# Performance work log

Hardware: AMD Instinct MI355X
Metric: run time of the kernel (lower is better)

Reference implementation:

```python
import jax, jax.numpy as jnp
import numpy as np

D_MODEL = 768
BATCH = 4096
RANK_DIST = [(4, 512), (8, 256), (16, 128), (32, 64), (64, 32)]


@jax.custom_vjp
def jumprelu(x):
    # hard threshold at 0 in fwd; full straight-through estimator in bwd
    return x * (x > 0.0).astype(x.dtype)


def _jr_fwd(x):
    return jumprelu(x), None


def _jr_bwd(res, g):
    return (g,)


jumprelu.defvjp(_jr_fwd, _jr_bwd)


def setup_inputs() -> dict:
    key = jax.random.key(0)
    keys = jax.random.split(key, 1 + 3 * len(RANK_DIST))
    inp = {"x": jax.random.normal(keys[0], (BATCH, D_MODEL), dtype=jnp.float32)}
    for i, (n, r) in enumerate(RANK_DIST):
        kV, kU, kE = keys[1 + 3 * i], keys[2 + 3 * i], keys[3 + 3 * i]
        scale = (1.0 / (D_MODEL * r)) ** 0.25
        inp[f"V{i}"] = scale * jax.random.normal(kV, (n, r, D_MODEL), dtype=jnp.float32)
        inp[f"U{i}"] = scale * jax.random.normal(kU, (n, D_MODEL, r), dtype=jnp.float32)
        enc = jax.random.normal(kE, (n, D_MODEL), dtype=jnp.float32)
        inp[f"enc{i}"] = enc / jnp.linalg.norm(enc, axis=1, keepdims=True)
        inp[f"b{i}"] = jnp.full((n,), -1.0, dtype=jnp.float32)
    return inp


def _group_forward(x, V, U, enc, b):
    n, r, d = V.shape
    pre = x @ enc.T - b                      # (b, n)
    gate = jumprelu(pre)                     # (b, n)
    Vx = jnp.einsum("nrd,bd->nbr", V, x)    # (n, b, r)
    # fused: UVx gated by gate then summed over transforms n
    out = jnp.einsum("ndr,nbr,bn->bd", U, Vx, gate)  # (b, d)
    u_norms = jnp.linalg.norm(U.reshape(n, -1), axis=1)
    v_norms = jnp.linalg.norm(V.reshape(n, -1), axis=1)
    frob = u_norms * v_norms / jnp.sqrt(jnp.asarray(d * r, dtype=x.dtype))
    return out, gate, frob


def reference(x, V0, U0, enc0, b0, V1, U1, enc1, b1, V2, U2, enc2, b2,
              V3, U3, enc3, b3, V4, U4, enc4, b4):
    Vs = [V0, V1, V2, V3, V4]
    Us = [U0, U1, U2, U3, U4]
    encs = [enc0, enc1, enc2, enc3, enc4]
    bs = [b0, b1, b2, b3, b4]
    output = jnp.zeros_like(x)
    total_sparsity = jnp.asarray(0.0, dtype=x.dtype)
    total_active = jnp.asarray(0.0, dtype=x.dtype)
    gate_acts = []
    for V, U, enc, b in zip(Vs, Us, encs, bs):
        g_out, gate, frob = _group_forward(x, V, U, enc, b)
        output = output + g_out
        mean_abs_gate = jnp.abs(gate).mean(axis=0)
        total_sparsity = total_sparsity + (jnp.tanh(mean_abs_gate) * frob).sum()
        total_active = total_active + (gate > 0).astype(x.dtype).sum(axis=1).mean()
        gate_acts.append(gate)
    return (output, total_sparsity, total_active, *gate_acts)
```

## Files before the change

kernel.cpp:

```cpp
#include <hip/hip_runtime.h>

#define BATCH 4096
#define DM 768
#define LTOT 10240
#define NG 124

typedef __bf16 bf16x8 __attribute__((ext_vector_type(8)));
typedef short short8 __attribute__((ext_vector_type(8)));
typedef float f32x4 __attribute__((ext_vector_type(4)));

struct Ptr5 { const float* p[5]; };

__device__ __forceinline__ unsigned short f2bf(float f) {
    unsigned u = __builtin_bit_cast(unsigned, f);
    unsigned r = (u + 0x7FFFu + ((u >> 16) & 1u)) >> 16;
    return (unsigned short)r;
}

__device__ __forceinline__ short8 pack8(float4 a, float4 b) {
    union { unsigned short u[8]; short8 s; } o;
    o.u[0] = f2bf(a.x); o.u[1] = f2bf(a.y); o.u[2] = f2bf(a.z); o.u[3] = f2bf(a.w);
    o.u[4] = f2bf(b.x); o.u[5] = f2bf(b.y); o.u[6] = f2bf(b.z); o.u[7] = f2bf(b.w);
    return o.s;
}


__global__ __launch_bounds__(256) void prep_k(const float* __restrict__ x,
                                              Ptr5 vp, Ptr5 up, Ptr5 ep, Ptr5 bp,
                                              unsigned short* __restrict__ vb,
                                              unsigned short* __restrict__ w2t,
                                              unsigned short* __restrict__ xb,
                                              float* __restrict__ gate_ws,
                                              float* __restrict__ outg,
                                              float* __restrict__ vslot,
                                              float* __restrict__ uslot,
                                              float* __restrict__ gslot,
                                              float* __restrict__ aslot) {
    const int basen[5] = {0, 4, 12, 28, 60};
    int bx = blockIdx.x;
    int tid = threadIdx.x;
    if (bx < 32) {
        __shared__ unsigned short lA[128 * 64];
        __shared__ unsigned short lB[128 * 64];
        __shared__ float sgs[128];
        __shared__ float sac;
        int wave = tid >> 6, lane = tid & 63;
        int wm = wave >> 1, wn = wave & 1;
        int lan15 = lane & 15, quad = lane >> 4;
        int sw = lan15 & 7;
        int m0 = bx * 128;
        f32x4 acc[4][4] = {};
        for (int k0 = 0; k0 < DM; k0 += 64) {
            __syncthreads();
            #pragma unroll
            for (int i = 0; i < 4; i++) {
                int gidx = i * 256 + tid;
                int row = gidx >> 3, kb = gidx & 7;
                int r7 = row & 7;
                int la = (row >> 3) * 512 + r7 * 64 + (kb ^ r7) * 8;
                int sidx = (m0 + row) * 192 + (k0 >> 2) + kb * 2;
                float4 a0 = ((const float4*)x)[sidx];
                float4 a1 = ((const float4*)x)[sidx + 1];
                *(short8*)(lA + la) = pack8(a0, a1);
                float4 b0 = {0.f, 0.f, 0.f, 0.f}, b1 = {0.f, 0.f, 0.f, 0.f};
                if (row < NG) {
                    int g = (row < 4) ? 0 : (row < 12) ? 1 : (row < 28) ? 2 :
                            (row < 60) ? 3 : 4;
                    int ni = row - basen[g];
                    int eidx = ni * 192 + (k0 >> 2) + kb * 2;
                    b0 = ((const float4*)ep.p[g])[eidx];
                    b1 = ((const float4*)ep.p[g])[eidx + 1];
                }
                *(short8*)(lB + la) = pack8(b0, b1);
            }
            __syncthreads();
            #pragma unroll
            for (int kk = 0; kk < 2; kk++) {
                int kb = kk * 4 + quad;
                int kel = (kb ^ sw) * 8;
                bf16x8 af[4], bfr[4];
                #pragma unroll
                for (int t = 0; t < 4; t++) {
                    short8 ra = *(const short8*)(lA + (wm * 64 + t * 16 + lan15) * 64 + kel);
                    short8 rb = *(const short8*)(lB + (wn * 64 + t * 16 + lan15) * 64 + kel);
                    af[t]  = __builtin_bit_cast(bf16x8, ra);
                    bfr[t] = __builtin_bit_cast(bf16x8, rb);
                }
                #pragma unroll
                for (int mt = 0; mt < 4; mt++)
                    #pragma unroll
                    for (int nt = 0; nt < 4; nt++)
                        acc[mt][nt] = __builtin_amdgcn_mfma_f32_16x16x32_bf16(
                            af[mt], bfr[nt], acc[mt][nt], 0, 0, 0);
            }
        }
        if (tid < 128) sgs[tid] = 0.f;
        if (tid == 0) sac = 0.f;
        __syncthreads();
        const size_t baseg[5] = {3145730ull, 3145730ull + 16384, 3145730ull + 49152,
                                 3145730ull + 114688, 3145730ull + 245760};
        float cnt = 0.f;
        #pragma unroll
        for (int nt = 0; nt < 4; nt++) {
            int col = wn * 64 + nt * 16 + lan15;
            float cs = 0.f;
            if (col < NG) {
                int g = (col < 4) ? 0 : (col < 12) ? 1 : (col < 28) ? 2 :
                        (col < 60) ? 3 : 4;
                int ni = col - basen[g];
                int w = 4 << g;
                float bv = bp.p[g][ni];
                #pragma unroll
                for (int mt = 0; mt < 4; mt++) {
                    int r0 = m0 + wm * 64 + mt * 16 + quad * 4;
                    #pragma unroll
                    for (int rg = 0; rg < 4; rg++) {
                        float pre = acc[mt][nt][rg] - bv;
                        float gt = pre > 0.f ? pre : 0.f;
                        gate_ws[(size_t)(r0 + rg) * NG + col] = gt;
                        outg[baseg[g] + (size_t)(r0 + rg) * w + ni] = gt;
                        cs += gt;
                        if (pre > 0.f) cnt += 1.f;
                    }
                }
                cs += __shfl_xor(cs, 16);
                cs += __shfl_xor(cs, 32);
                if (quad == 0) atomicAdd(&sgs[col], cs);
            }
        }
        #pragma unroll
        for (int off = 32; off > 0; off >>= 1) cnt += __shfl_xor(cnt, off);
        if (lane == 0) atomicAdd(&sac, cnt);
        __syncthreads();
        if (tid < NG) gslot[bx * NG + tid] = sgs[tid];
        if (tid == 0) aslot[bx] = sac;
    } else if (bx < 1952) {
        __shared__ float swave[4];
        int cb = bx - 32;
        int isV = cb < 960;
        int wb = isV ? cb : cb - 960;
        int g = wb / 192;
        int within = wb - g * 192;
        const float* src = isV ? vp.p[g] : up.p[g];
        int r = 512 >> g, lr = 9 - g;
        float ss = 0.f;
        #pragma unroll
        for (int i = 0; i < 8; i++) {
            int j = within * 2048 + i * 256 + tid;
            float4 v = ((const float4*)src)[j];
            ss += v.x*v.x + v.y*v.y + v.z*v.z + v.w*v.w;
            ushort4 o;
            o.x = f2bf(v.x); o.y = f2bf(v.y); o.z = f2bf(v.z); o.w = f2bf(v.w);
            if (isV) {
                ((ushort4*)vb)[(size_t)(g * 192 + within) * 2048 + i * 256 + tid] = o;
            } else {
                int idx = j * 4;
                int rr = idx & (r - 1);
                int t2 = idx >> lr;
                int d  = t2 % DM;
                int n  = t2 / DM;
                size_t dst = (size_t)d * LTOT + (size_t)(g << 11) + (size_t)n * r + rr;
                *(ushort4*)(w2t + dst) = o;
            }
        }
        #pragma unroll
        for (int off = 32; off > 0; off >>= 1) ss += __shfl_down(ss, off);
        if ((tid & 63) == 0) swave[tid >> 6] = ss;
        __syncthreads();
        if (tid == 0) {
            float t = (swave[0] + swave[1]) + (swave[2] + swave[3]);
            (isV ? vslot : uslot)[wb] = t;
        }
    } else {
        int base = (bx - 1952) * 2048;
        #pragma unroll
        for (int i = 0; i < 8; i++) {
            int j = base + i * 256 + tid;
            float4 v = ((const float4*)x)[j];
            ushort4 o;
            o.x = f2bf(v.x); o.y = f2bf(v.y); o.z = f2bf(v.z); o.w = f2bf(v.w);
            ((ushort4*)xb)[j] = o;
        }
    }
}

template <int ROWS, int NT>
__device__ __forceinline__ void stage(const unsigned short* __restrict__ src, int ld,
                                      unsigned short* lds, int wv, int lane) {
    int rsub = lane >> 3;
    int colb = ((lane ^ rsub) & 7) * 8;
    #pragma unroll
    for (int i = 0; i < ROWS * 8 / NT; i++) {
        int c = i * (NT / 64) + wv;
        const unsigned short* gp = src + (size_t)(c * 8 + rsub) * ld + colb;
        __builtin_amdgcn_global_load_lds((const __attribute__((address_space(1))) void*)gp,
                                         (__attribute__((address_space(3))) void*)(lds + c * 512),
                                         16, 0, 0);
    }
}

template <int BM, int BN, int NT>
__global__ __launch_bounds__(NT) void gemm_nt(const unsigned short* __restrict__ A,
                                              const unsigned short* __restrict__ Bm,
                                              int Kblk, int lda, int ldb,
                                              void* __restrict__ Cout,
                                              const float* __restrict__ gate, int ldc) {
    __shared__ unsigned short lA[BM * 64];
    __shared__ unsigned short lB[BN * 64];
    int tid = threadIdx.x, wave = tid >> 6, lane = tid & 63;
    constexpr int WN = BN / 64;
    int wm = wave / WN, wn = wave % WN;
    int m0 = blockIdx.x * BM, n0 = blockIdx.y * BN;
    A  += (size_t)m0 * lda;
    Bm += (size_t)n0 * ldb;
    f32x4 acc[4][4] = {};
    int lan15 = lane & 15, quad = lane >> 4;
    int sw = lan15 & 7;

    for (int k0 = 0; k0 < Kblk; k0 += 64) {
        stage<BM, NT>(A + k0, lda, lA, wave, lane);
        stage<BN, NT>(Bm + k0, ldb, lB, wave, lane);
        __syncthreads();
        #pragma unroll
        for (int kk = 0; kk < 2; kk++) {
            int kb = kk * 4 + quad;
            int kel = (kb ^ sw) * 8;
            bf16x8 af[4], bfr[4];
            #pragma unroll
            for (int t = 0; t < 4; t++) {
                short8 ra = *(const short8*)(lA + (size_t)(wm * 64 + t * 16 + lan15) * 64 + kel);
                short8 rb = *(const short8*)(lB + (size_t)(wn * 64 + t * 16 + lan15) * 64 + kel);
                af[t]  = __builtin_bit_cast(bf16x8, ra);
                bfr[t] = __builtin_bit_cast(bf16x8, rb);
            }
            #pragma unroll
            for (int mt = 0; mt < 4; mt++)
                #pragma unroll
                for (int nt = 0; nt < 4; nt++)
                    acc[mt][nt] = __builtin_amdgcn_mfma_f32_16x16x32_bf16(af[mt], bfr[nt],
                                                                          acc[mt][nt], 0, 0, 0);
        }
        __syncthreads();
    }

    const int basen[5] = {0, 4, 12, 28, 60};
    unsigned short* H = (unsigned short*)Cout;
    #pragma unroll
    for (int mt = 0; mt < 4; mt++) {
        __syncthreads();
        #pragma unroll
        for (int nt = 0; nt < 4; nt++) {
            int col = n0 + wn * 64 + nt * 16 + lan15;
            int g = col >> 11;
            int ngl = basen[g] + ((col & 2047) >> (9 - g));
            #pragma unroll
            for (int rg = 0; rg < 4; rg++) {
                int grow = m0 + wm * 64 + mt * 16 + quad * 4 + rg;
                float gv = gate[(size_t)grow * NG + ngl];
                lA[wave * 1024 + (quad * 4 + rg) * 64 + nt * 16 + lan15] =
                    f2bf(acc[mt][nt][rg] * gv);
            }
        }
        __syncthreads();
        #pragma unroll
        for (int i = 0; i < 2; i++) {
            int f = i * NT + tid;
            int R = f >> 5;
            int u = f & 31;
            int wv2 = ((R >> 4) << 2) + (u >> 3);
            short8 vread = *(const short8*)(lA + wv2 * 1024 + (R & 15) * 64 + (u & 7) * 8);
            int grow = m0 + (R >> 4) * 64 + mt * 16 + (R & 15);
            *(short8*)(H + (size_t)grow * ldc + n0 + u * 8) = vread;
        }
    }
}

__global__ __launch_bounds__(256, 2) void gemm2_nt(const unsigned short* __restrict__ A,
                                                   const unsigned short* __restrict__ Bm,
                                                   float* __restrict__ P) {
    __shared__ unsigned short lA[2][256 * 32];
    __shared__ unsigned short lB[2][128 * 32];
    int tid = threadIdx.x, wave = tid >> 6, lane = tid & 63;
    int wm = wave >> 1, wn = wave & 1;
    int lan15 = lane & 15, quad = lane >> 4;
    int kel = (quad ^ (lan15 & 3)) * 8;
    int m0 = blockIdx.x * 256, n0 = blockIdx.y * 128;
    const unsigned short* Ab = A  + (size_t)m0 * LTOT + (size_t)blockIdx.z * 2048;
    const unsigned short* Bb = Bm + (size_t)n0 * LTOT + (size_t)blockIdx.z * 2048;
    int rsub = lane >> 2;
    int gofs = ((lane & 3) ^ (rsub & 3)) * 8;

#define G2_STA(cur, kof, c) __builtin_amdgcn_global_load_lds( \
        (const __attribute__((address_space(1))) void*)(Ab + (size_t)((c) * 16 + rsub) * LTOT + (kof) + gofs), \
        (__attribute__((address_space(3))) void*)(&lA[cur][(c) * 512]), 16, 0, 0)
#define G2_STB(cur, kof, c) __builtin_amdgcn_global_load_lds( \
        (const __attribute__((address_space(1))) void*)(Bb + (size_t)((c) * 16 + rsub) * LTOT + (kof) + gofs), \
        (__attribute__((address_space(3))) void*)(&lB[cur][(c) * 512]), 16, 0, 0)

    f32x4 acc[8][4] = {};
    G2_STA(0, 0, wave); G2_STA(0, 0, wave + 8); G2_STB(0, 0, wave); G2_STB(0, 0, wave + 4);
    G2_STA(0, 0, wave + 4); G2_STA(0, 0, wave + 12);

#define G2_TILE(cur, knext) { \
    asm volatile("s_waitcnt vmcnt(2)" ::: "memory"); \
    __builtin_amdgcn_s_barrier(); \
    asm volatile("" ::: "memory"); \
    G2_STA(cur ^ 1, knext, wave); G2_STA(cur ^ 1, knext, wave + 8); \
    G2_STB(cur ^ 1, knext, wave); G2_STB(cur ^ 1, knext, wave + 4); \
    bf16x8 bfr[4], af[4]; \
    _Pragma("unroll") for (int nt = 0; nt < 4; nt++) \
        bfr[nt] = __builtin_bit_cast(bf16x8, *(const short8*)(&lB[cur][(wn * 64 + nt * 16 + lan15) * 32 + kel])); \
    _Pragma("unroll") for (int mt = 0; mt < 4; mt++) \
        af[mt] = __builtin_bit_cast(bf16x8, *(const short8*)(&lA[cur][(wm * 128 + mt * 16 + lan15) * 32 + kel])); \
    __builtin_amdgcn_s_setprio(1); \
    _Pragma("unroll") for (int mt = 0; mt < 4; mt++) \
        _Pragma("unroll") for (int nt = 0; nt < 4; nt++) \
            acc[mt][nt] = __builtin_amdgcn_mfma_f32_16x16x32_bf16(af[mt], bfr[nt], acc[mt][nt], 0, 0, 0); \
    __builtin_amdgcn_s_setprio(0); \
    asm volatile("s_waitcnt vmcnt(4)" ::: "memory"); \
    __builtin_amdgcn_s_barrier(); \
    asm volatile("" ::: "memory"); \
    G2_STA(cur ^ 1, knext, wave + 4); G2_STA(cur ^ 1, knext, wave + 12); \
    _Pragma("unroll") for (int mt = 0; mt < 4; mt++) \
        af[mt] = __builtin_bit_cast(bf16x8, *(const short8*)(&lA[cur][(wm * 128 + 64 + mt * 16 + lan15) * 32 + kel])); \
    __builtin_amdgcn_s_setprio(1); \
    _Pragma("unroll") for (int mt = 0; mt < 4; mt++) \
        _Pragma("unroll") for (int nt = 0; nt < 4; nt++) \
            acc[4 + mt][nt] = __builtin_amdgcn_mfma_f32_16x16x32_bf16(af[mt], bfr[nt], acc[4 + mt][nt], 0, 0, 0); \
    __builtin_amdgcn_s_setprio(0); \
}

    for (int t2 = 0; t2 < 32; t2++) {
        int k0 = t2 * 64;
        G2_TILE(0, k0 + 32);
        int knext = (t2 == 31) ? (k0 + 32) : (k0 + 64);
        G2_TILE(1, knext);
    }
#undef G2_TILE
#undef G2_STA
#undef G2_STB
    asm volatile("s_waitcnt vmcnt(0)" ::: "memory");

    float* Pz = P + (size_t)blockIdx.z * ((size_t)BATCH * DM);
    #pragma unroll
    for (int mt = 0; mt < 8; mt++) {
        #pragma unroll
        for (int rg = 0; rg < 4; rg++) {
            int row = m0 + wm * 128 + mt * 16 + quad * 4 + rg;
            float* pr = Pz + (size_t)row * DM + n0 + wn * 64 + lan15;
            #pragma unroll
            for (int nt = 0; nt < 4; nt++)
                pr[nt * 16] = acc[mt][nt][rg];
        }
    }
}


__global__ __launch_bounds__(256) void reduce_k(const float4* __restrict__ P,
                                                float4* __restrict__ out, int quarter,
                                                const float* __restrict__ vslot,
                                                const float* __restrict__ uslot,
                                                const float* __restrict__ gslot,
                                                const float* __restrict__ aslot,
                                                float* __restrict__ o2) {
    int i = blockIdx.x * 256 + threadIdx.x;
    float4 a = P[i], b = P[i + quarter], c = P[i + 2 * quarter], d = P[i + 3 * quarter];
    float4 e = P[i + 4 * quarter];
    float4 o;
    o.x = ((a.x + b.x) + (c.x + d.x)) + e.x;
    o.y = ((a.y + b.y) + (c.y + d.y)) + e.y;
    o.z = ((a.z + b.z) + (c.z + d.z)) + e.z;
    o.w = ((a.w + b.w) + (c.w + d.w)) + e.w;
    out[i] = o;
    if (blockIdx.x == 0) {
        __shared__ float sh[128];
        const int basen[5] = {0, 4, 12, 28, 60};
        int t = threadIdx.x;
        if (t < 128) {
            float v = 0.f;
            if (t < NG) {
                int g = (t < 4) ? 0 : (t < 12) ? 1 : (t < 28) ? 2 : (t < 60) ? 3 : 4;
                int nloc = t - basen[g];
                int bpseg = 48 >> g;
                float vs = 0.f, us = 0.f;
                int base = g * 192 + nloc * bpseg;
                for (int j = 0; j < bpseg; j++) { vs += vslot[base + j]; us += uslot[base + j]; }
                float gs = 0.f;
                for (int bb = 0; bb < 32; bb++) gs += gslot[bb * NG + t];
                float rr = (float)(512 >> g);
                float mean = gs * (1.0f / BATCH);
                float frob = sqrtf(us * vs) / sqrtf(768.0f * rr);
                v = tanhf(mean) * frob;
            }
            sh[t] = v;
        }
        if (t == 128) {
            float asum = 0.f;
            for (int bb = 0; bb < 32; bb++) asum += aslot[bb];
            o2[1] = asum * (1.0f / BATCH);
        }
        __syncthreads();
        for (int s = 64; s > 0; s >>= 1) {
            if (threadIdx.x < s) sh[threadIdx.x] += sh[threadIdx.x + s];
            __syncthreads();
        }
        if (threadIdx.x == 0) o2[0] = sh[0];
    }
}


extern "C" void kernel_launch(void* const* d_in, const int* in_sizes, int n_in,
                              void* d_out, int out_size, void* d_ws, size_t ws_size,
                              hipStream_t stream) {
    const float* x = (const float*)d_in[0];
    Ptr5 vp, up, ep, bp;
    for (int g = 0; g < 5; g++) {
        vp.p[g] = (const float*)d_in[1 + 4 * g];
        up.p[g] = (const float*)d_in[2 + 4 * g];
        ep.p[g] = (const float*)d_in[3 + 4 * g];
        bp.p[g] = (const float*)d_in[4 + 4 * g];
    }
    float* out = (float*)d_out;
    char* ws = (char*)d_ws;
    size_t off = 0;
    unsigned short* w2t  = (unsigned short*)(ws + off); off += (size_t)LTOT * DM * 2;
    float* vslot         = (float*)(ws + off);          off += 960 * 4;
    float* uslot         = (float*)(ws + off);          off += 960 * 4;
    float* gslot         = (float*)(ws + off);          off += 32 * NG * 4;
    float* aslot         = (float*)(ws + off);          off += 32 * 4 + 256;
    unsigned short* Hg   = (unsigned short*)(ws + off); off += (size_t)BATCH * LTOT * 2;
    float* partial       = (float*)(ws + off);          off += 5ull * BATCH * DM * 4;
    unsigned short* xb      = (unsigned short*)partial;
    unsigned short* vb      = (unsigned short*)((char*)partial + (size_t)BATCH * DM * 2);
    float* gate_ws          = (float*)((char*)partial + (size_t)BATCH * DM * 2
                                                      + (size_t)LTOT * DM * 2);

    prep_k<<<dim3(2336), 256, 0, stream>>>(
        x, vp, up, ep, bp, vb, w2t, xb, gate_ws, out,
        vslot, uslot, gslot, aslot);

    gemm_nt<128, 256, 512><<<dim3(BATCH / 128, LTOT / 256, 1), 512, 0, stream>>>(
        xb, vb, DM, DM, DM, (void*)Hg, gate_ws, LTOT);
    gemm2_nt<<<dim3(BATCH / 256, DM / 128, 5), 256, 0, stream>>>(Hg, w2t, partial);
    reduce_k<<<dim3(BATCH * DM / 4 / 256), 256, 0, stream>>>(
        (const float4*)partial, (float4*)out, BATCH * DM / 4,
        vslot, uslot, gslot, aslot, out + (size_t)BATCH * DM);
}
```

Before: 347.0 us.

## Enlarge gemm2 tile to 256x256 with 8 waves and deeper LDS pipeline

Rewrites the second GEMM (Hg times w2t) to use 256x256 output tiles per block with 512 threads instead of 256x128 with 256 threads. A 128KB LDS region holds four k-chunks of A and B in flight, giving a deeper prefetch schedule with a new swizzle. The larger tile increases operand reuse and cuts global traffic for A, but it halves the grid (16x3x5 = 240 blocks) and drops to one block per CU, which may hurt occupancy and load balance.

```diff
diff --git a/kernel.cpp b/kernel.cpp
--- a/kernel.cpp
+++ b/kernel.cpp
@@ -275,82 +275,100 @@
     }
 }
 
-__global__ __launch_bounds__(256, 2) void gemm2_nt(const unsigned short* __restrict__ A,
+__global__ __launch_bounds__(512, 1) void gemm2_nt(const unsigned short* __restrict__ A,
                                                    const unsigned short* __restrict__ Bm,
                                                    float* __restrict__ P) {
-    __shared__ unsigned short lA[2][256 * 32];
-    __shared__ unsigned short lB[2][128 * 32];
-    int tid = threadIdx.x, wave = tid >> 6, lane = tid & 63;
-    int wm = wave >> 1, wn = wave & 1;
-    int lan15 = lane & 15, quad = lane >> 4;
-    int kel = (quad ^ (lan15 & 3)) * 8;
-    int m0 = blockIdx.x * 256, n0 = blockIdx.y * 128;
-    const unsigned short* Ab = A  + (size_t)m0 * LTOT + (size_t)blockIdx.z * 2048;
-    const unsigned short* Bb = Bm + (size_t)n0 * LTOT + (size_t)blockIdx.z * 2048;
-    int rsub = lane >> 2;
-    int gofs = ((lane & 3) ^ (rsub & 3)) * 8;
-
-#define G2_STA(cur, kof, c) __builtin_amdgcn_global_load_lds( \
-        (const __attribute__((address_space(1))) void*)(Ab + (size_t)((c) * 16 + rsub) * LTOT + (kof) + gofs), \
-        (__attribute__((address_space(3))) void*)(&lA[cur][(c) * 512]), 16, 0, 0)
-#define G2_STB(cur, kof, c) __builtin_amdgcn_global_load_lds( \
-        (const __attribute__((address_space(1))) void*)(Bb + (size_t)((c) * 16 + rsub) * LTOT + (kof) + gofs), \
-        (__attribute__((address_space(3))) void*)(&lB[cur][(c) * 512]), 16, 0, 0)
+    __shared__ unsigned short lds[65536];
+    const int tid = threadIdx.x;
+    const int wave = tid >> 6, lane = tid & 63;
+    const int wm = wave >> 2, wn = wave & 3;
+    const int lan15 = lane & 15, quad = lane >> 4;
+    const int swz = quad ^ ((lan15 >> 1) & 3);
+    const int m0 = blockIdx.x * 256, n0 = blockIdx.y * 256;
+    const unsigned short* Ab = A  + (size_t)m0 * LTOT + blockIdx.z * 2048;
+    const unsigned short* Bb = Bm + (size_t)n0 * LTOT + blockIdx.z * 2048;
+    const int srow = lane >> 2;
+    const int sgr  = (lane & 3) ^ ((lane >> 3) & 3);
+    const int rdA = (wm * 128 + lan15) * 32 + swz * 8;
+    const int rdB = 32768 + (wn * 64 + lan15) * 32 + swz * 8;
+
+#define STG(base_us, gb, koff) do { \
+    const unsigned short* _s0 = (gb) + (size_t)(wave * 16 + srow) * LTOT + (koff) + sgr * 8; \
+    const unsigned short* _s1 = (gb) + (size_t)((wave + 8) * 16 + srow) * LTOT + (koff) + sgr * 8; \
+    __builtin_amdgcn_global_load_lds((const __attribute__((address_space(1))) void*)_s0, \
+        (__attribute__((address_space(3))) void*)(lds + (base_us) + wave * 512), 16, 0, 0); \
+    __builtin_amdgcn_global_load_lds((const __attribute__((address_space(1))) void*)_s1, \
+        (__attribute__((address_space(3))) void*)(lds + (base_us) + (wave + 8) * 512), 16, 0, 0); \
+} while (0)
+#define STGA(buf, kh, koff) STG(((buf) * 2 + (kh)) * 8192, Ab, koff)
+#define STGB(buf, kh, koff) STG(32768 + ((buf) * 2 + (kh)) * 8192, Bb, koff)
+
+#define RDA(msub, bufkg) { \
+    _Pragma("unroll") for (int t = 0; t < 4; t++) \
+        af[t] = __builtin_bit_cast(bf16x8, \
+            *(const short8*)(lds + (bufkg) * 8192 + rdA + ((msub) * 64 + t * 16) * 32)); }
+#define RDB(bufkg) { \
+    _Pragma("unroll") for (int t = 0; t < 4; t++) \
+        bf[t] = __builtin_bit_cast(bf16x8, \
+            *(const short8*)(lds + 32768 + (bufkg) * 8192 + rdB - 32768 + t * 512)); }
+#define SYNC1 do { __builtin_amdgcn_s_barrier(); \
+    asm volatile("s_waitcnt lgkmcnt(0)" ::: "memory"); \
+    __builtin_amdgcn_sched_barrier(0); } while (0)
+#define MM(msub) do { __builtin_amdgcn_s_setprio(1); \
+    _Pragma("unroll") for (int mt = 0; mt < 4; mt++) \
+        _Pragma("unroll") for (int nf = 0; nf < 4; nf++) \
+            acc[(msub) * 4 + mt][nf] = __builtin_amdgcn_mfma_f32_16x16x32_bf16( \
+                af[mt], bf[nf], acc[(msub) * 4 + mt][nf], 0, 0, 0); \
+    __builtin_amdgcn_s_setprio(0); } while (0)
+#define SYNC2 do { asm volatile("" ::: "memory"); __builtin_amdgcn_s_barrier(); \
+    asm volatile("" ::: "memory"); } while (0)
 
     f32x4 acc[8][4] = {};
-    G2_STA(0, 0, wave); G2_STA(0, 0, wave + 8); G2_STB(0, 0, wave); G2_STB(0, 0, wave + 4);
-    G2_STA(0, 0, wave + 4); G2_STA(0, 0, wave + 12);
-
-#define G2_TILE(cur, knext) { \
-    asm volatile("s_waitcnt vmcnt(2)" ::: "memory"); \
-    __builtin_amdgcn_s_barrier(); \
-    asm volatile("" ::: "memory"); \
-    G2_STA(cur ^ 1, knext, wave); G2_STA(cur ^ 1, knext, wave + 8); \
-    G2_STB(cur ^ 1, knext, wave); G2_STB(cur ^ 1, knext, wave + 4); \
-    bf16x8 bfr[4], af[4]; \
-    _Pragma("unroll") for (int nt = 0; nt < 4; nt++) \
-        bfr[nt] = __builtin_bit_cast(bf16x8, *(const short8*)(&lB[cur][(wn * 64 + nt * 16 + lan15) * 32 + kel])); \
-    _Pragma("unroll") for (int mt = 0; mt < 4; mt++) \
-        af[mt] = __builtin_bit_cast(bf16x8, *(const short8*)(&lA[cur][(wm * 128 + mt * 16 + lan15) * 32 + kel])); \
-    __builtin_amdgcn_s_setprio(1); \
-    _Pragma("unroll") for (int mt = 0; mt < 4; mt++) \
-        _Pragma("unroll") for (int nt = 0; nt < 4; nt++) \
-            acc[mt][nt] = __builtin_amdgcn_mfma_f32_16x16x32_bf16(af[mt], bfr[nt], acc[mt][nt], 0, 0, 0); \
-    __builtin_amdgcn_s_setprio(0); \
-    asm volatile("s_waitcnt vmcnt(4)" ::: "memory"); \
-    __builtin_amdgcn_s_barrier(); \
-    asm volatile("" ::: "memory"); \
-    G2_STA(cur ^ 1, knext, wave + 4); G2_STA(cur ^ 1, knext, wave + 12); \
-    _Pragma("unroll") for (int mt = 0; mt < 4; mt++) \
-        af[mt] = __builtin_bit_cast(bf16x8, *(const short8*)(&lA[cur][(wm * 128 + 64 + mt * 16 + lan15) * 32 + kel])); \
-    __builtin_amdgcn_s_setprio(1); \
-    _Pragma("unroll") for (int mt = 0; mt < 4; mt++) \
-        _Pragma("unroll") for (int nt = 0; nt < 4; nt++) \
-            acc[4 + mt][nt] = __builtin_amdgcn_mfma_f32_16x16x32_bf16(af[mt], bfr[nt], acc[4 + mt][nt], 0, 0, 0); \
-    __builtin_amdgcn_s_setprio(0); \
-}
-
-    for (int t2 = 0; t2 < 32; t2++) {
-        int k0 = t2 * 64;
-        G2_TILE(0, k0 + 32);
-        int knext = (t2 == 31) ? (k0 + 32) : (k0 + 64);
-        G2_TILE(1, knext);
-    }
-#undef G2_TILE
-#undef G2_STA
-#undef G2_STB
+    STGA(0, 0, 0);  STGB(0, 0, 0);
+    STGA(0, 1, 32); STGB(0, 1, 32);
+    STGA(1, 0, 64); STGB(1, 0, 64);
+    STGB(1, 1, 96);
+    asm volatile("s_waitcnt vmcnt(10)" ::: "memory");
+    __builtin_amdgcn_s_barrier();
+
+    for (int i = 0; i < 32; i++) {
+        const int buf = i & 1;
+        bf16x8 af[4], bf[4];
+        RDA(0, buf * 2 + 0); RDB(buf * 2 + 0);
+        if (i + 1 < 32) STGA(buf ^ 1, 1, (i + 1) * 64 + 32);
+        SYNC1; MM(0); SYNC2;
+        RDA(1, buf * 2 + 0);
+        if (i + 2 < 32) STGB(buf, 0, (i + 2) * 64);
+        SYNC1; MM(1);
+        asm volatile("s_waitcnt vmcnt(6)" ::: "memory");
+        SYNC2;
+        RDA(0, buf * 2 + 1); RDB(buf * 2 + 1);
+        if (i + 2 < 32) STGA(buf, 0, (i + 2) * 64);
+        SYNC1; MM(0); SYNC2;
+        RDA(1, buf * 2 + 1);
+        if (i + 2 < 32) STGB(buf, 1, (i + 2) * 64 + 32);
+        SYNC1; MM(1); SYNC2;
+    }
     asm volatile("s_waitcnt vmcnt(0)" ::: "memory");
+#undef STG
+#undef STGA
+#undef STGB
+#undef RDA
+#undef RDB
+#undef SYNC1
+#undef SYNC2
+#undef MM
 
     float* Pz = P + (size_t)blockIdx.z * ((size_t)BATCH * DM);
     #pragma unroll
-    for (int mt = 0; mt < 8; mt++) {
+    for (int mf = 0; mf < 8; mf++) {
         #pragma unroll
         for (int rg = 0; rg < 4; rg++) {
-            int row = m0 + wm * 128 + mt * 16 + quad * 4 + rg;
+            int row = m0 + wm * 128 + mf * 16 + quad * 4 + rg;
             float* pr = Pz + (size_t)row * DM + n0 + wn * 64 + lan15;
             #pragma unroll
-            for (int nt = 0; nt < 4; nt++)
-                pr[nt * 16] = acc[mt][nt][rg];
+            for (int nf = 0; nf < 4; nf++)
+                pr[nf * 16] = acc[mf][nf][rg];
         }
     }
 }
@@ -441,7 +459,7 @@
 
     gemm_nt<128, 256, 512><<<dim3(BATCH / 128, LTOT / 256, 1), 512, 0, stream>>>(
         xb, vb, DM, DM, DM, (void*)Hg, gate_ws, LTOT);
-    gemm2_nt<<<dim3(BATCH / 256, DM / 128, 5), 256, 0, stream>>>(Hg, w2t, partial);
+    gemm2_nt<<<dim3(BATCH / 256, DM / 256, 5), 512, 0, stream>>>(Hg, w2t, partial);
     reduce_k<<<dim3(BATCH * DM / 4 / 256), 256, 0, stream>>>(
         (const float4*)partial, (float4*)out, BATCH * DM / 4,
         vslot, uslot, gslot, aslot, out + (size_t)BATCH * DM);
```

Result: faster. 329.6 us (-5.0%).
